# Optimization experiments

Measured on AMD Instinct MI355X. Metric: run time of the kernel, lower is better.

## Reference

```python
import jax, jax.numpy as jnp
import numpy as np

E = 8        # n_experts
TOP_K = 2    # n_activated_experts
B, T, C = 4, 2048, 2048   # batch, seq, d_model
F = 5632     # expert FFN hidden (SwiGLU)


def setup_inputs() -> dict:
    key = jax.random.key(0)
    k = jax.random.split(key, 5)
    s = 0.02  # init scale keeps activations sane
    return {
        "x":  jax.random.normal(k[0], (B, T, C), jnp.float32),
        "Wg": jax.random.normal(k[1], (C, E), jnp.float32) * s,   # gate Linear (no bias)
        "W1": jax.random.normal(k[2], (E, C, F), jnp.float32) * s, # expert gate proj
        "W3": jax.random.normal(k[3], (E, C, F), jnp.float32) * s, # expert up proj
        "W2": jax.random.normal(k[4], (E, F, C), jnp.float32) * s, # expert down proj
    }


def _moe(x, Wg, W1, W3, W2, top_k=TOP_K, norm_probs=True):
    Bb, Tt, Cc = x.shape
    xf = x.reshape(-1, Cc)                                   # [N, C]
    logits = xf @ Wg                                         # [N, E]
    probs = jax.nn.softmax(logits.astype(jnp.float32), axis=-1)
    probs, indices = jax.lax.top_k(probs, top_k)             # [N, K]
    if norm_probs:
        probs = probs / probs.sum(axis=-1, keepdims=True)
    probs = probs.astype(x.dtype)
    N, Ee = xf.shape[0], W1.shape[0]
    # per-token combine weights: w[n, e] = prob if expert e selected for token n else 0
    # (top_k indices are distinct per token, so at most one add per (n, e))
    w = jnp.zeros((N, Ee), x.dtype).at[jnp.arange(N)[:, None], indices].add(probs)
    # scan over experts: weight-0 tokens contribute nothing, matching the sparse
    # masked dispatch/scatter-add of the original exactly.
    def body(y, ws):
        w1, w3, w2, we = ws                                   # we: [N]
        h = jax.nn.silu(xf @ w1) * (xf @ w3)                  # [N, F]
        return y + we[:, None] * (h @ w2), None
    y, _ = jax.lax.scan(body, jnp.zeros_like(xf), (W1, W3, W2, w.T))
    return y.reshape(Bb, Tt, Cc)


def reference(x, Wg, W1, W3, W2):
    return _moe(x, Wg, W1, W3, W2)
```

## Files before the change

### kernel.cpp

```cpp
#include <hip/hip_runtime.h>

#define N_TOK 8192
#define C_DIM 2048
#define F_DIM 5632
#define E_NUM 8
#define BK 64

#define BM 256
#define MAXT 72
#define BN1 128
#define GRID1 (MAXT * (F_DIM/BN1))
#define BN2 256
#define KSPLIT 2
#define GRID2 (MAXT * (C_DIM/BN2) * KSPLIT)
#define NT1 (C_DIM/BK)
#define NT2H (F_DIM/BK/KSPLIT)
#define KHALF (F_DIM/KSPLIT)

#define PRE_R 2048
#define PRE_Y 4096
#define PRE_T 45056
#define GRID_PRE (PRE_R + PRE_Y + PRE_T)

typedef __attribute__((ext_vector_type(8))) short bf16x8;
typedef __attribute__((ext_vector_type(4))) float f32x4;

typedef const void __attribute__((address_space(1)))* gas1;
typedef void __attribute__((address_space(3)))* las3;

__device__ __forceinline__ unsigned short f2bf(float f){
  union { float f; unsigned u; } v; v.f = f;
  unsigned r = v.u + 0x7FFFu + ((v.u >> 16) & 1u);
  return (unsigned short)(r >> 16);
}

__device__ __forceinline__ void glds16(const unsigned short* g, unsigned short* l){
  __builtin_amdgcn_global_load_lds((gas1)g, (las3)l, 16, 0, 0);
}

#define MFMA_BF16 __builtin_amdgcn_mfma_f32_16x16x32_bf16

#define BAR1_VM(N) do{ asm volatile("s_waitcnt vmcnt(" #N ")" ::: "memory"); \
    __builtin_amdgcn_sched_barrier(0); __builtin_amdgcn_s_barrier(); \
    __builtin_amdgcn_sched_barrier(0); } while(0)
#define BAR2() do{ asm volatile("s_waitcnt lgkmcnt(0)" ::: "memory"); \
    __builtin_amdgcn_sched_barrier(0); __builtin_amdgcn_s_barrier(); \
    __builtin_amdgcn_sched_barrier(0); } while(0)

__global__ __launch_bounds__(256) void k_pre(
    const float* __restrict__ x, const float* __restrict__ Wg,
    const float* __restrict__ W1, const float* __restrict__ W3,
    int* __restrict__ cnt, int* __restrict__ list, float* __restrict__ p_slot,
    unsigned short* __restrict__ xb, unsigned short* __restrict__ wb13,
    float* __restrict__ y)
{
  __shared__ float t[64][65];
  int bid = blockIdx.x;
  int tid = threadIdx.x;

  if (bid < PRE_R){
    int wid = tid >> 6, lane = tid & 63;
    int n = bid * 4 + wid;
    int e = lane >> 3, sub = lane & 7;
    const float* xr = x + (size_t)n * C_DIM;
    float acc = 0.f;
    for (int i0 = sub*4; i0 < C_DIM; i0 += 32){
      float4 v = *(const float4*)&xr[i0];
      acc += v.x * Wg[(i0  )*E_NUM + e];
      acc += v.y * Wg[(i0+1)*E_NUM + e];
      acc += v.z * Wg[(i0+2)*E_NUM + e];
      acc += v.w * Wg[(i0+3)*E_NUM + e];
    }
    acc += __shfl_xor(acc, 1);
    acc += __shfl_xor(acc, 2);
    acc += __shfl_xor(acc, 4);
    float lg[E_NUM];
    #pragma unroll
    for (int j = 0; j < E_NUM; ++j) lg[j] = __shfl(acc, j*8);
    unsigned short* xbr = xb + (size_t)n * C_DIM;
    #pragma unroll
    for (int i0 = lane*4; i0 < C_DIM; i0 += 256){
      float4 v = *(const float4*)&xr[i0];
      ushort4 u; u.x = f2bf(v.x); u.y = f2bf(v.y); u.z = f2bf(v.z); u.w = f2bf(v.w);
      *(ushort4*)&xbr[i0] = u;
    }
    if (lane == 0){
      int e1 = 0; float m1 = lg[0];
      #pragma unroll
      for (int j = 1; j < E_NUM; ++j) if (lg[j] > m1){ m1 = lg[j]; e1 = j; }
      int e2 = -1; float m2 = -1e30f;
      #pragma unroll
      for (int j = 0; j < E_NUM; ++j) if (j != e1 && lg[j] > m2){ m2 = lg[j]; e2 = j; }
      float p1 = 1.f / (1.f + __expf(m2 - m1));
      float p2 = 1.f - p1;
      int pos1 = atomicAdd(&cnt[e1], 1);
      list[e1*N_TOK + pos1] = n*2;
      p_slot[n*2] = p1;
      int pos2 = atomicAdd(&cnt[e2], 1);
      list[e2*N_TOK + pos2] = n*2 + 1;
      p_slot[n*2 + 1] = p2;
    }
    return;
  }
  if (bid < PRE_R + PRE_Y){
    float4* y4 = (float4*)y;
    size_t base = (size_t)(bid - PRE_R) * 1024 + tid;
    float4 z4 = {0.f, 0.f, 0.f, 0.f};
    #pragma unroll
    for (int j = 0; j < 4; ++j) y4[base + j*256] = z4;
    return;
  }
  int rel = bid - (PRE_R + PRE_Y);
  int z = rel / 2816;
  int r2 = rel - z*2816;
  int fx = r2 % 88, cy = r2 / 88;
  const float* in = ((z < 8) ? W1 : W3) + (size_t)(z & 7) * C_DIM * F_DIM;
  unsigned short* out = wb13 + (size_t)z * C_DIM * F_DIM;
  int c0 = fx*64, r0 = cy*64;
  int tx = tid & 63, ty = tid >> 6;
  #pragma unroll
  for (int i = 0; i < 16; ++i){
    int r = ty + i*4;
    t[r][tx] = in[(size_t)(r0 + r) * F_DIM + c0 + tx];
  }
  __syncthreads();
  #pragma unroll
  for (int i = 0; i < 16; ++i){
    int cr = ty + i*4;
    out[(size_t)(c0 + cr) * C_DIM + r0 + tx] = f2bf(t[tx][cr]);
  }
}

__global__ void k_tw2(const float* __restrict__ W2, unsigned short* __restrict__ wb2){
  __shared__ float t[64][65];
  const float* in = W2 + (size_t)blockIdx.z * F_DIM * C_DIM;
  unsigned short* out = wb2 + (size_t)blockIdx.z * C_DIM * F_DIM;
  int c0 = blockIdx.x * 64, r0 = blockIdx.y * 64;
  int tx = threadIdx.x, ty = threadIdx.y;
  #pragma unroll
  for (int i = 0; i < 16; ++i){
    int r = ty + i*4;
    t[r][tx] = in[(size_t)(r0 + r) * C_DIM + c0 + tx];
  }
  __syncthreads();
  #pragma unroll
  for (int i = 0; i < 16; ++i){
    int cr = ty + i*4;
    out[(size_t)(c0 + cr) * F_DIM + r0 + tx] = f2bf(t[tx][cr]);
  }
}

__global__ void k_prefix(const int* __restrict__ cnt, int* __restrict__ meta){
  if (threadIdx.x == 0 && blockIdx.x == 0){
    int acc = 0, t = 0;
    for (int e = 0; e < E_NUM; ++e){
      meta[e] = acc; acc += cnt[e];
      int nt = (cnt[e] + BM - 1) / BM;
      for (int i = 0; i < nt; ++i) meta[16 + t++] = (e << 16) | i;
    }
    meta[8] = t;
  }
}

__global__ __launch_bounds__(512, 2) void k_gemm1(
    const unsigned short* __restrict__ xb,
    const unsigned short* __restrict__ wb1,
    const unsigned short* __restrict__ wb3,
    unsigned short* __restrict__ h,
    const int* __restrict__ cnt,
    const int* __restrict__ meta,
    const int* __restrict__ list)
{
  __shared__ __align__(16) unsigned short lds[2*32768];
  int o = blockIdx.x;
  int tid = threadIdx.x;

  int w = (o & 7) * (GRID1/8) + (o >> 3);
  int t = w % MAXT;
  int n0 = (w / MAXT) * BN1;
  if (t >= meta[8]) return;
  int info = meta[16 + t];
  int e  = info >> 16;
  int m0 = (info & 0xffff) * BM;
  int count = cnt[e];
  int hbase = meta[e];

  int lane = tid & 63, wid = tid >> 6;
  int wm = wid >> 1, wn = wid & 1;
  int l15 = lane & 15;
  int xc0 = (lane >> 4) ^ (lane & 7);
  int xc1 = xc0 ^ 4;

  int srow = tid >> 3;
  int swz = ((tid & 7) ^ (srow & 7)) * 8;
  const unsigned short* aP[4];
  #pragma unroll
  for (int u = 0; u < 4; ++u){
    int ts = list[e*N_TOK + m0 + u*64 + srow];
    int tok = (ts >> 1) & (N_TOK - 1);
    aP[u] = xb + (size_t)tok * C_DIM + swz;
  }
  const unsigned short* bP[4];
  #pragma unroll
  for (int u = 0; u < 4; ++u){
    const unsigned short* base = (u < 2) ? wb1 : wb3;
    bP[u] = base + ((size_t)e*F_DIM + n0 + (u & 1)*64 + srow) * C_DIM + swz;
  }
  int ldw = wid * 512;

  #define ST_A(u, kt) glds16(aP[u] + (kt)*BK, &lds[((kt)&1)*32768 + (u)*4096 + ldw])
  #define ST_B(u, kt) glds16(bP[u] + (kt)*BK, &lds[((kt)&1)*32768 + 16384 + (u)*4096 + ldw])
  #define READ_A(d, buf) do{ _Pragma("unroll") for (int m_ = 0; m_ < 4; ++m_){ \
      int row_ = wm*64 + m_*16 + l15; \
      d[m_][0] = *(const bf16x8*)&(buf)[row_*64 + xc0*8]; \
      d[m_][1] = *(const bf16x8*)&(buf)[row_*64 + xc1*8]; } }while(0)
  #define READ_B(d1, d3, buf, q) do{ int brow_ = wn*64 + (q)*16 + l15; \
      d1[0] = *(const bf16x8*)&(buf)[16384 + brow_*64 + xc0*8]; \
      d1[1] = *(const bf16x8*)&(buf)[16384 + brow_*64 + xc1*8]; \
      d3[0] = *(const bf16x8*)&(buf)[24576 + brow_*64 + xc0*8]; \
      d3[1] = *(const bf16x8*)&(buf)[24576 + brow_*64 + xc1*8]; }while(0)
  #define MFMA16(q, b1, b3) do{ _Pragma("unroll") for (int m_ = 0; m_ < 4; ++m_){ \
      acc1[m_][q] = MFMA_BF16(a[m_][0], b1[0], acc1[m_][q], 0, 0, 0); \
      acc1[m_][q] = MFMA_BF16(a[m_][1], b1[1], acc1[m_][q], 0, 0, 0); \
      acc3[m_][q] = MFMA_BF16(a[m_][0], b3[0], acc3[m_][q], 0, 0, 0); \
      acc3[m_][q] = MFMA_BF16(a[m_][1], b3[1], acc3[m_][q], 0, 0, 0); } }while(0)

  ST_A(0,0); ST_A(1,0); ST_A(2,0); ST_A(3,0);
  ST_B(0,0); ST_B(1,0); ST_B(2,0); ST_B(3,0);
  ST_A(0,1); ST_A(1,1); ST_A(2,1); ST_A(3,1);
  asm volatile("s_waitcnt vmcnt(4)" ::: "memory");
  __builtin_amdgcn_sched_barrier(0);
  __builtin_amdgcn_s_barrier();
  __builtin_amdgcn_sched_barrier(0);

  f32x4 zero = {0.f, 0.f, 0.f, 0.f};
  f32x4 acc1[4][4], acc3[4][4];
  #pragma unroll
  for (int m = 0; m < 4; ++m)
    #pragma unroll
    for (int q = 0; q < 4; ++q){ acc1[m][q] = zero; acc3[m][q] = zero; }

  bf16x8 a[4][2];
  READ_A(a, lds);
  bf16x8 bX1[2], bX3[2], bY1[2], bY3[2];
  READ_B(bX1, bX3, lds, 0);

  for (int kt = 0; kt < NT1; ++kt){
    const unsigned short* bufc = &lds[(kt & 1)*32768];
    const unsigned short* bufn = &lds[((kt+1) & 1)*32768];
    ST_B(0, kt+1); ST_B(1, kt+1); ST_B(2, kt+1); ST_B(3, kt+1);
    READ_B(bY1, bY3, bufc, 1);
    __builtin_amdgcn_s_setprio(1);
    MFMA16(0, bX1, bX3);
    __builtin_amdgcn_s_setprio(0);
    ST_A(0, kt+2); ST_A(1, kt+2);
    READ_B(bX1, bX3, bufc, 2);
    __builtin_amdgcn_s_setprio(1);
    MFMA16(1, bY1, bY3);
    __builtin_amdgcn_s_setprio(0);
    ST_A(2, kt+2); ST_A(3, kt+2);
    READ_B(bY1, bY3, bufc, 3);
    __builtin_amdgcn_s_setprio(1);
    MFMA16(2, bX1, bX3);
    __builtin_amdgcn_s_setprio(0);
    BAR1_VM(4);
    bf16x8 an[4][2];
    READ_A(an, bufn);
    READ_B(bX1, bX3, bufn, 0);
    __builtin_amdgcn_s_setprio(1);
    MFMA16(3, bY1, bY3);
    __builtin_amdgcn_s_setprio(0);
    BAR2();
    #pragma unroll
    for (int m = 0; m < 4; ++m){ a[m][0] = an[m][0]; a[m][1] = an[m][1]; }
  }
  asm volatile("s_waitcnt vmcnt(0)" ::: "memory");

  #pragma unroll
  for (int m = 0; m < 4; ++m){
    #pragma unroll
    for (int r = 0; r < 4; ++r){
      int rloc = m0 + wm*64 + m*16 + ((lane >> 4) * 4) + r;
      if (rloc < count){
        unsigned short* hrow = h + (size_t)(hbase + rloc) * F_DIM + n0 + wn*64 + l15;
        #pragma unroll
        for (int q = 0; q < 4; ++q){
          float v1 = acc1[m][q][r];
          float v3 = acc3[m][q][r];
          float hv = (v1 / (1.f + __expf(-v1))) * v3;
          hrow[q*16] = f2bf(hv);
        }
      }
    }
  }
  #undef ST_A
  #undef ST_B
  #undef READ_A
  #undef READ_B
  #undef MFMA16
}

__global__ __launch_bounds__(512, 2) void k_gemm2(
    const unsigned short* __restrict__ h,
    const unsigned short* __restrict__ wb2,
    float* __restrict__ y,
    const int* __restrict__ cnt,
    const int* __restrict__ meta,
    const int* __restrict__ list,
    const float* __restrict__ p_slot)
{
  int o = blockIdx.x;
  int w = (o & 7) * (GRID2/8) + (o >> 3);
  int ks = w / (GRID2/KSPLIT);
  int r2 = w % (GRID2/KSPLIT);
  int t = r2 % MAXT;
  int n0 = (r2 / MAXT) * BN2;
  if (t >= meta[8]) return;
  int info = meta[16 + t];
  int e  = info >> 16;
  int m0 = (info & 0xffff) * BM;
  int count = cnt[e];
  int hbase = meta[e];

  __shared__ __align__(16) unsigned short lds[2*32768];

  int tid = threadIdx.x;
  int lane = tid & 63, wid = tid >> 6;
  int wm = wid >> 1, wn = wid & 1;
  int l15 = lane & 15;
  int xc0 = (lane >> 4) ^ (lane & 7);
  int xc1 = xc0 ^ 4;

  int srow = tid >> 3;
  int swz = ((tid & 7) ^ (srow & 7)) * 8;
  size_t kb0 = (size_t)ks * KHALF;
  const unsigned short* aP[4];
  #pragma unroll
  for (int u = 0; u < 4; ++u)
    aP[u] = h + (size_t)(hbase + m0 + u*64 + srow) * F_DIM + kb0 + swz;
  const unsigned short* bP[4];
  #pragma unroll
  for (int u = 0; u < 4; ++u)
    bP[u] = wb2 + ((size_t)e*C_DIM + n0 + u*64 + srow) * F_DIM + kb0 + swz;
  int ldw = wid * 512;

  #define ST_A2(u, kt) glds16(aP[u] + (kt)*BK, &lds[((kt)&1)*32768 + (u)*4096 + ldw])
  #define ST_B2(u, kt) glds16(bP[u] + (kt)*BK, &lds[((kt)&1)*32768 + 16384 + (u)*4096 + ldw])
  #define READ_A2(d, buf) do{ _Pragma("unroll") for (int m_ = 0; m_ < 4; ++m_){ \
      int row_ = wm*64 + m_*16 + l15; \
      d[m_][0] = *(const bf16x8*)&(buf)[row_*64 + xc0*8]; \
      d[m_][1] = *(const bf16x8*)&(buf)[row_*64 + xc1*8]; } }while(0)
  #define READ_B2(d, buf, q) do{ _Pragma("unroll") for (int j_ = 0; j_ < 2; ++j_){ \
      int brow_ = wn*128 + ((q)*2 + j_)*16 + l15; \
      d[j_][0] = *(const bf16x8*)&(buf)[16384 + brow_*64 + xc0*8]; \
      d[j_][1] = *(const bf16x8*)&(buf)[16384 + brow_*64 + xc1*8]; } }while(0)
  #define MFMA2(qb, d) do{ _Pragma("unroll") for (int m_ = 0; m_ < 4; ++m_) \
      _Pragma("unroll") for (int j_ = 0; j_ < 2; ++j_){ \
        acc[m_][(qb)*2+j_] = MFMA_BF16(a[m_][0], d[j_][0], acc[m_][(qb)*2+j_], 0, 0, 0); \
        acc[m_][(qb)*2+j_] = MFMA_BF16(a[m_][1], d[j_][1], acc[m_][(qb)*2+j_], 0, 0, 0); } }while(0)

  ST_A2(0,0); ST_A2(1,0); ST_A2(2,0); ST_A2(3,0);
  ST_B2(0,0); ST_B2(1,0); ST_B2(2,0); ST_B2(3,0);
  asm volatile("s_waitcnt vmcnt(4)" ::: "memory");
  ST_A2(0,1); ST_A2(1,1); ST_A2(2,1); ST_A2(3,1);
  ST_B2(0,1); ST_B2(2,1);
  asm volatile("s_waitcnt vmcnt(6)" ::: "memory");
  __builtin_amdgcn_sched_barrier(0);
  __builtin_amdgcn_s_barrier();
  __builtin_amdgcn_sched_barrier(0);

  f32x4 zero = {0.f, 0.f, 0.f, 0.f};
  f32x4 acc[4][8];
  #pragma unroll
  for (int m = 0; m < 4; ++m)
    #pragma unroll
    for (int nf = 0; nf < 8; ++nf) acc[m][nf] = zero;

  bf16x8 a[4][2];
  READ_A2(a, lds);
  bf16x8 bfX[2][2], bfY[2][2];
  READ_B2(bfX, lds, 0);

  for (int kt = 0; kt < NT2H; ++kt){
    const unsigned short* bufc = &lds[(kt & 1)*32768];
    const unsigned short* bufn = &lds[((kt+1) & 1)*32768];
    ST_B2(1, kt+1); ST_B2(3, kt+1);
    READ_B2(bfY, bufc, 1);
    __builtin_amdgcn_s_setprio(1);
    MFMA2(0, bfX);
    __builtin_amdgcn_s_setprio(0);
    ST_A2(0, kt+2); ST_A2(1, kt+2);
    READ_B2(bfX, bufc, 2);
    __builtin_amdgcn_s_setprio(1);
    MFMA2(1, bfY);
    __builtin_amdgcn_s_setprio(0);
    ST_A2(2, kt+2); ST_A2(3, kt+2);
    READ_B2(bfY, bufc, 3);
    __builtin_amdgcn_s_setprio(1);
    MFMA2(2, bfX);
    __builtin_amdgcn_s_setprio(0);
    ST_B2(0, kt+2); ST_B2(2, kt+2);
    BAR1_VM(6);
    bf16x8 an[4][2];
    READ_A2(an, bufn);
    READ_B2(bfX, bufn, 0);
    __builtin_amdgcn_s_setprio(1);
    MFMA2(3, bfY);
    __builtin_amdgcn_s_setprio(0);
    BAR2();
    #pragma unroll
    for (int m = 0; m < 4; ++m){ a[m][0] = an[m][0]; a[m][1] = an[m][1]; }
  }
  asm volatile("s_waitcnt vmcnt(0)" ::: "memory");

  #pragma unroll
  for (int m = 0; m < 4; ++m){
    #pragma unroll
    for (int r = 0; r < 4; ++r){
      int rloc = m0 + wm*64 + m*16 + ((lane >> 4) * 4) + r;
      if (rloc < count){
        int ts = list[e*N_TOK + rloc];
        float p = p_slot[ts];
        int tok = ts >> 1;
        float* yr = y + (size_t)tok * C_DIM + n0 + wn*128 + l15;
        #pragma unroll
        for (int nf = 0; nf < 8; ++nf)
          atomicAdd(&yr[nf*16], p * acc[m][nf][r]);
      }
    }
  }
  #undef ST_A2
  #undef ST_B2
  #undef READ_A2
  #undef READ_B2
  #undef MFMA2
}

extern "C" void kernel_launch(void* const* d_in, const int* in_sizes, int n_in,
                              void* d_out, int out_size, void* d_ws, size_t ws_size,
                              hipStream_t stream)
{
  const float* x  = (const float*)d_in[0];
  const float* Wg = (const float*)d_in[1];
  const float* W1 = (const float*)d_in[2];
  const float* W3 = (const float*)d_in[3];
  const float* W2 = (const float*)d_in[4];
  float* y = (float*)d_out;
  (void)in_sizes; (void)n_in; (void)out_size; (void)ws_size;

  char* ws = (char*)d_ws;
  size_t o = 0;
  auto alloc = [&](size_t bytes)->char* {
    char* p = ws + o;
    o = (o + bytes + 255) & ~(size_t)255;
    return p;
  };
  int*    cnt    = (int*)  alloc(E_NUM * 4);
  int*    meta   = (int*)  alloc(160 * 4);
  float*  p_slot = (float*)alloc((size_t)2*N_TOK * 4);
  int*    list   = (int*)  alloc((size_t)E_NUM*N_TOK * 4);
  unsigned short* xb  = (unsigned short*)alloc((size_t)N_TOK*C_DIM * 2);
  unsigned short* wb1 = (unsigned short*)alloc((size_t)E_NUM*C_DIM*F_DIM * 2);
  unsigned short* wb3 = (unsigned short*)alloc((size_t)E_NUM*C_DIM*F_DIM * 2);
  unsigned short* wb2 = (unsigned short*)alloc((size_t)E_NUM*C_DIM*F_DIM * 2);
  unsigned short* h   = (unsigned short*)alloc((size_t)(2*N_TOK + 1024)*F_DIM * 2);
  (void)wb3;

  hipMemsetAsync(cnt, 0, E_NUM * 4, stream);
  k_pre<<<GRID_PRE, 256, 0, stream>>>(x, Wg, W1, W3, cnt, list, p_slot, xb, wb1, y);
  k_prefix<<<1, 64, 0, stream>>>(cnt, meta);
  k_tw2<<<dim3(C_DIM/64, F_DIM/64, E_NUM), dim3(64,4), 0, stream>>>(W2, wb2);
  k_gemm1<<<GRID1, 512, 0, stream>>>(xb, wb1, wb3, h, cnt, meta, list);
  k_gemm2<<<GRID2, 512, 0, stream>>>(h, wb2, y, cnt, meta, list, p_slot);
}
```

Baseline: 1.807 ms.

## Triple-buffer B tiles in gemm1 LDS to prefetch weights two steps ahead

Changes the LDS layout of the gate/up GEMM so A stays double-buffered while the W1/W3 B tiles move into a three-slot ring buffer, with B loads issued two k-steps ahead. The goal is to hide global-load latency for the weight stream better by keeping more loads in flight, with the vmcnt waits adjusted to match. LDS per block grows from 128KB to 160KB, which at 512 threads with launch bounds of 2 may cut occupancy to one block per CU. The workspace buffers are padded to cover the prefetch reading past the end.

New measurement: 1.854 ms. 2.6% more time.

```diff
diff --git a/kernel.cpp b/kernel.cpp
--- a/kernel.cpp
+++ b/kernel.cpp
@@ -171,7 +171,7 @@
     const int* __restrict__ meta,
     const int* __restrict__ list)
 {
-  __shared__ __align__(16) unsigned short lds[2*32768];
+  __shared__ __align__(16) unsigned short lds[81920];
   int o = blockIdx.x;
   int tid = threadIdx.x;
 
@@ -200,25 +200,28 @@
     int tok = (ts >> 1) & (N_TOK - 1);
     aP[u] = xb + (size_t)tok * C_DIM + swz;
   }
-  const unsigned short* bP[4];
-  #pragma unroll
-  for (int u = 0; u < 4; ++u){
-    const unsigned short* base = (u < 2) ? wb1 : wb3;
-    bP[u] = base + ((size_t)e*F_DIM + n0 + (u & 1)*64 + srow) * C_DIM + swz;
+  const unsigned short* b1P[2];
+  const unsigned short* b3P[2];
+  #pragma unroll
+  for (int u = 0; u < 2; ++u){
+    b1P[u] = wb1 + ((size_t)e*F_DIM + n0 + u*64 + srow) * C_DIM + swz;
+    b3P[u] = wb3 + ((size_t)e*F_DIM + n0 + u*64 + srow) * C_DIM + swz;
   }
   int ldw = wid * 512;
 
-  #define ST_A(u, kt) glds16(aP[u] + (kt)*BK, &lds[((kt)&1)*32768 + (u)*4096 + ldw])
-  #define ST_B(u, kt) glds16(bP[u] + (kt)*BK, &lds[((kt)&1)*32768 + 16384 + (u)*4096 + ldw])
-  #define READ_A(d, buf) do{ _Pragma("unroll") for (int m_ = 0; m_ < 4; ++m_){ \
+  #define ST_A(u, kt)      glds16(aP[u]  + (kt)*BK, &lds[((kt)&1)*16384 + (u)*4096 + ldw])
+  #define ST_B(u, kt, sl)  do{ \
+      glds16(b1P[u] + (kt)*BK, &lds[32768 + (sl)*8192 + (u)*4096 + ldw]); \
+      glds16(b3P[u] + (kt)*BK, &lds[57344 + (sl)*8192 + (u)*4096 + ldw]); }while(0)
+  #define READ_A(d, ab) do{ _Pragma("unroll") for (int m_ = 0; m_ < 4; ++m_){ \
       int row_ = wm*64 + m_*16 + l15; \
-      d[m_][0] = *(const bf16x8*)&(buf)[row_*64 + xc0*8]; \
-      d[m_][1] = *(const bf16x8*)&(buf)[row_*64 + xc1*8]; } }while(0)
-  #define READ_B(d1, d3, buf, q) do{ int brow_ = wn*64 + (q)*16 + l15; \
-      d1[0] = *(const bf16x8*)&(buf)[16384 + brow_*64 + xc0*8]; \
-      d1[1] = *(const bf16x8*)&(buf)[16384 + brow_*64 + xc1*8]; \
-      d3[0] = *(const bf16x8*)&(buf)[24576 + brow_*64 + xc0*8]; \
-      d3[1] = *(const bf16x8*)&(buf)[24576 + brow_*64 + xc1*8]; }while(0)
+      d[m_][0] = *(const bf16x8*)&lds[(ab) + row_*64 + xc0*8]; \
+      d[m_][1] = *(const bf16x8*)&lds[(ab) + row_*64 + xc1*8]; } }while(0)
+  #define READ_B(d1, d3, sl, q) do{ int brow_ = wn*64 + (q)*16 + l15; \
+      d1[0] = *(const bf16x8*)&lds[32768 + (sl)*8192 + brow_*64 + xc0*8]; \
+      d1[1] = *(const bf16x8*)&lds[32768 + (sl)*8192 + brow_*64 + xc1*8]; \
+      d3[0] = *(const bf16x8*)&lds[57344 + (sl)*8192 + brow_*64 + xc0*8]; \
+      d3[1] = *(const bf16x8*)&lds[57344 + (sl)*8192 + brow_*64 + xc1*8]; }while(0)
   #define MFMA16(q, b1, b3) do{ _Pragma("unroll") for (int m_ = 0; m_ < 4; ++m_){ \
       acc1[m_][q] = MFMA_BF16(a[m_][0], b1[0], acc1[m_][q], 0, 0, 0); \
       acc1[m_][q] = MFMA_BF16(a[m_][1], b1[1], acc1[m_][q], 0, 0, 0); \
@@ -226,9 +229,10 @@
       acc3[m_][q] = MFMA_BF16(a[m_][1], b3[1], acc3[m_][q], 0, 0, 0); } }while(0)
 
   ST_A(0,0); ST_A(1,0); ST_A(2,0); ST_A(3,0);
-  ST_B(0,0); ST_B(1,0); ST_B(2,0); ST_B(3,0);
+  ST_B(0,0,0); ST_B(1,0,0);
   ST_A(0,1); ST_A(1,1); ST_A(2,1); ST_A(3,1);
-  asm volatile("s_waitcnt vmcnt(4)" ::: "memory");
+  ST_B(0,1,1); ST_B(1,1,1);
+  asm volatile("s_waitcnt vmcnt(8)" ::: "memory");
   __builtin_amdgcn_sched_barrier(0);
   __builtin_amdgcn_s_barrier();
   __builtin_amdgcn_sched_barrier(0);
@@ -241,38 +245,39 @@
     for (int q = 0; q < 4; ++q){ acc1[m][q] = zero; acc3[m][q] = zero; }
 
   bf16x8 a[4][2];
-  READ_A(a, lds);
+  READ_A(a, 0);
   bf16x8 bX1[2], bX3[2], bY1[2], bY3[2];
-  READ_B(bX1, bX3, lds, 0);
-
+  READ_B(bX1, bX3, 0, 0);
+
+  int s0 = 0, s1 = 1, s2 = 2;
   for (int kt = 0; kt < NT1; ++kt){
-    const unsigned short* bufc = &lds[(kt & 1)*32768];
-    const unsigned short* bufn = &lds[((kt+1) & 1)*32768];
-    ST_B(0, kt+1); ST_B(1, kt+1); ST_B(2, kt+1); ST_B(3, kt+1);
-    READ_B(bY1, bY3, bufc, 1);
+    int abn = ((kt+1)&1)*16384;
+    ST_B(0, kt+2, s2); ST_B(1, kt+2, s2);
+    READ_B(bY1, bY3, s0, 1);
     __builtin_amdgcn_s_setprio(1);
     MFMA16(0, bX1, bX3);
     __builtin_amdgcn_s_setprio(0);
     ST_A(0, kt+2); ST_A(1, kt+2);
-    READ_B(bX1, bX3, bufc, 2);
+    READ_B(bX1, bX3, s0, 2);
     __builtin_amdgcn_s_setprio(1);
     MFMA16(1, bY1, bY3);
     __builtin_amdgcn_s_setprio(0);
     ST_A(2, kt+2); ST_A(3, kt+2);
-    READ_B(bY1, bY3, bufc, 3);
+    READ_B(bY1, bY3, s0, 3);
     __builtin_amdgcn_s_setprio(1);
     MFMA16(2, bX1, bX3);
     __builtin_amdgcn_s_setprio(0);
-    BAR1_VM(4);
+    BAR1_VM(8);
     bf16x8 an[4][2];
-    READ_A(an, bufn);
-    READ_B(bX1, bX3, bufn, 0);
+    READ_A(an, abn);
+    READ_B(bX1, bX3, s1, 0);
     __builtin_amdgcn_s_setprio(1);
     MFMA16(3, bY1, bY3);
     __builtin_amdgcn_s_setprio(0);
     BAR2();
     #pragma unroll
     for (int m = 0; m < 4; ++m){ a[m][0] = an[m][0]; a[m][1] = an[m][1]; }
+    int tmp = s0; s0 = s1; s1 = s2; s2 = tmp;
   }
   asm volatile("s_waitcnt vmcnt(0)" ::: "memory");
 
@@ -459,11 +464,11 @@
   int*    meta   = (int*)  alloc(160 * 4);
   float*  p_slot = (float*)alloc((size_t)2*N_TOK * 4);
   int*    list   = (int*)  alloc((size_t)E_NUM*N_TOK * 4);
-  unsigned short* xb  = (unsigned short*)alloc((size_t)N_TOK*C_DIM * 2);
+  unsigned short* xb  = (unsigned short*)alloc((size_t)N_TOK*C_DIM * 2 + 65536);
   unsigned short* wb1 = (unsigned short*)alloc((size_t)E_NUM*C_DIM*F_DIM * 2);
   unsigned short* wb3 = (unsigned short*)alloc((size_t)E_NUM*C_DIM*F_DIM * 2);
   unsigned short* wb2 = (unsigned short*)alloc((size_t)E_NUM*C_DIM*F_DIM * 2);
-  unsigned short* h   = (unsigned short*)alloc((size_t)(2*N_TOK + 1024)*F_DIM * 2);
+  unsigned short* h   = (unsigned short*)alloc((size_t)(2*N_TOK + 1024)*F_DIM * 2 + 65536);
   (void)wb3;
 
   hipMemsetAsync(cnt, 0, E_NUM * 4, stream);
```

## Replace atomic scatter-add in down-projection with bf16 slot buffer and combine kernel

Applied to the files above, without the earlier changes.

The down-projection GEMM no longer zeroes y and atomically adds weighted fp32 results per token. Instead it writes unweighted bf16 partials per (k-split, token-slot) into a dedicated buffer. A new combine kernel then sums the two k-split halves for both expert slots, applies the routing probabilities, and writes y once. This removes fp32 atomic traffic and the zero-fill pass. The cost is an extra kernel launch, a large intermediate buffer, and bf16 rounding of the partial sums.

Result: faster. 1.697 ms (-6.1%).

```diff
diff --git a/kernel.cpp b/kernel.cpp
--- a/kernel.cpp
+++ b/kernel.cpp
@@ -18,9 +18,8 @@
 #define KHALF (F_DIM/KSPLIT)
 
 #define PRE_R 2048
-#define PRE_Y 4096
 #define PRE_T 45056
-#define GRID_PRE (PRE_R + PRE_Y + PRE_T)
+#define GRID_PRE (PRE_R + PRE_T)
 
 typedef __attribute__((ext_vector_type(8))) short bf16x8;
 typedef __attribute__((ext_vector_type(4))) float f32x4;
@@ -51,8 +50,7 @@
     const float* __restrict__ x, const float* __restrict__ Wg,
     const float* __restrict__ W1, const float* __restrict__ W3,
     int* __restrict__ cnt, int* __restrict__ list, float* __restrict__ p_slot,
-    unsigned short* __restrict__ xb, unsigned short* __restrict__ wb13,
-    float* __restrict__ y)
+    unsigned short* __restrict__ xb, unsigned short* __restrict__ wb13)
 {
   __shared__ float t[64][65];
   int bid = blockIdx.x;
@@ -102,15 +100,7 @@
     }
     return;
   }
-  if (bid < PRE_R + PRE_Y){
-    float4* y4 = (float4*)y;
-    size_t base = (size_t)(bid - PRE_R) * 1024 + tid;
-    float4 z4 = {0.f, 0.f, 0.f, 0.f};
-    #pragma unroll
-    for (int j = 0; j < 4; ++j) y4[base + j*256] = z4;
-    return;
-  }
-  int rel = bid - (PRE_R + PRE_Y);
+  int rel = bid - PRE_R;
   int z = rel / 2816;
   int r2 = rel - z*2816;
   int fx = r2 % 88, cy = r2 / 88;
@@ -303,11 +293,10 @@
 __global__ __launch_bounds__(512, 2) void k_gemm2(
     const unsigned short* __restrict__ h,
     const unsigned short* __restrict__ wb2,
-    float* __restrict__ y,
+    unsigned short* __restrict__ ybuf,
     const int* __restrict__ cnt,
     const int* __restrict__ meta,
-    const int* __restrict__ list,
-    const float* __restrict__ p_slot)
+    const int* __restrict__ list)
 {
   int o = blockIdx.x;
   int w = (o & 7) * (GRID2/8) + (o >> 3);
@@ -420,12 +409,10 @@
       int rloc = m0 + wm*64 + m*16 + ((lane >> 4) * 4) + r;
       if (rloc < count){
         int ts = list[e*N_TOK + rloc];
-        float p = p_slot[ts];
-        int tok = ts >> 1;
-        float* yr = y + (size_t)tok * C_DIM + n0 + wn*128 + l15;
+        unsigned short* yr = ybuf + ((size_t)ks*(2*N_TOK) + ts)*C_DIM + n0 + wn*128 + l15;
         #pragma unroll
         for (int nf = 0; nf < 8; ++nf)
-          atomicAdd(&yr[nf*16], p * acc[m][nf][r]);
+          yr[nf*16] = f2bf(acc[m][nf][r]);
       }
     }
   }
@@ -434,6 +421,46 @@
   #undef READ_A2
   #undef READ_B2
   #undef MFMA2
+}
+
+__global__ __launch_bounds__(256) void k_combine(
+    const unsigned short* __restrict__ ybuf,
+    const float* __restrict__ p_slot,
+    float* __restrict__ y)
+{
+  const int CW = C_DIM/8;
+  int i = blockIdx.x * blockDim.x + threadIdx.x;
+  int stride = gridDim.x * blockDim.x;
+  const size_t KS_OFF = (size_t)(2*N_TOK) * C_DIM;
+  for (; i < N_TOK*CW; i += stride){
+    int n = i >> 8;
+    int c0 = (i & 255) * 8;
+    size_t b1 = (size_t)(2*n)   * C_DIM + c0;
+    size_t b2 = (size_t)(2*n+1) * C_DIM + c0;
+    ushort4 a0 = *(const ushort4*)&ybuf[b1];
+    ushort4 a1 = *(const ushort4*)&ybuf[b1+4];
+    ushort4 a2 = *(const ushort4*)&ybuf[KS_OFF + b1];
+    ushort4 a3 = *(const ushort4*)&ybuf[KS_OFF + b1+4];
+    ushort4 c2 = *(const ushort4*)&ybuf[b2];
+    ushort4 c3 = *(const ushort4*)&ybuf[b2+4];
+    ushort4 d2 = *(const ushort4*)&ybuf[KS_OFF + b2];
+    ushort4 d3 = *(const ushort4*)&ybuf[KS_OFF + b2+4];
+    float p1 = p_slot[2*n], p2 = p_slot[2*n+1];
+    float out[8];
+    #define B2F(u) __builtin_bit_cast(float, (unsigned)(u) << 16)
+    out[0] = p1*(B2F(a0.x)+B2F(a2.x)) + p2*(B2F(c2.x)+B2F(d2.x));
+    out[1] = p1*(B2F(a0.y)+B2F(a2.y)) + p2*(B2F(c2.y)+B2F(d2.y));
+    out[2] = p1*(B2F(a0.z)+B2F(a2.z)) + p2*(B2F(c2.z)+B2F(d2.z));
+    out[3] = p1*(B2F(a0.w)+B2F(a2.w)) + p2*(B2F(c2.w)+B2F(d2.w));
+    out[4] = p1*(B2F(a1.x)+B2F(a3.x)) + p2*(B2F(c3.x)+B2F(d3.x));
+    out[5] = p1*(B2F(a1.y)+B2F(a3.y)) + p2*(B2F(c3.y)+B2F(d3.y));
+    out[6] = p1*(B2F(a1.z)+B2F(a3.z)) + p2*(B2F(c3.z)+B2F(d3.z));
+    out[7] = p1*(B2F(a1.w)+B2F(a3.w)) + p2*(B2F(c3.w)+B2F(d3.w));
+    #undef B2F
+    float4* yo = (float4*)&y[(size_t)n * C_DIM + c0];
+    yo[0] = *(float4*)&out[0];
+    yo[1] = *(float4*)&out[4];
+  }
 }
 
 extern "C" void kernel_launch(void* const* d_in, const int* in_sizes, int n_in,
@@ -459,17 +486,19 @@
   int*    meta   = (int*)  alloc(160 * 4);
   float*  p_slot = (float*)alloc((size_t)2*N_TOK * 4);
   int*    list   = (int*)  alloc((size_t)E_NUM*N_TOK * 4);
-  unsigned short* xb  = (unsigned short*)alloc((size_t)N_TOK*C_DIM * 2);
+  unsigned short* xb  = (unsigned short*)alloc((size_t)N_TOK*C_DIM * 2 + 65536);
   unsigned short* wb1 = (unsigned short*)alloc((size_t)E_NUM*C_DIM*F_DIM * 2);
   unsigned short* wb3 = (unsigned short*)alloc((size_t)E_NUM*C_DIM*F_DIM * 2);
   unsigned short* wb2 = (unsigned short*)alloc((size_t)E_NUM*C_DIM*F_DIM * 2);
-  unsigned short* h   = (unsigned short*)alloc((size_t)(2*N_TOK + 1024)*F_DIM * 2);
+  unsigned short* h   = (unsigned short*)alloc((size_t)(2*N_TOK + 1024)*F_DIM * 2 + 65536);
+  unsigned short* ybuf= (unsigned short*)alloc((size_t)KSPLIT*2*N_TOK*C_DIM * 2);
   (void)wb3;
 
   hipMemsetAsync(cnt, 0, E_NUM * 4, stream);
-  k_pre<<<GRID_PRE, 256, 0, stream>>>(x, Wg, W1, W3, cnt, list, p_slot, xb, wb1, y);
+  k_pre<<<GRID_PRE, 256, 0, stream>>>(x, Wg, W1, W3, cnt, list, p_slot, xb, wb1);
   k_prefix<<<1, 64, 0, stream>>>(cnt, meta);
   k_tw2<<<dim3(C_DIM/64, F_DIM/64, E_NUM), dim3(64,4), 0, stream>>>(W2, wb2);
   k_gemm1<<<GRID1, 512, 0, stream>>>(xb, wb1, wb3, h, cnt, meta, list);
-  k_gemm2<<<GRID2, 512, 0, stream>>>(h, wb2, y, cnt, meta, list, p_slot);
-}
+  k_gemm2<<<GRID2, 512, 0, stream>>>(h, wb2, ybuf, cnt, meta, list);
+  k_combine<<<4096, 256, 0, stream>>>(ybuf, p_slot, y);
+}
```
